# Optimization experiments

Hardware: AMD Instinct MI355X
Metric: run time of the kernel (lower is better)

## Reference

```python
import jax, jax.numpy as jnp
import numpy as np

# dims
N_USER = 30000; N_ITEM = 30000; HID = 256; HEADS = 4; DH = HID // HEADS
L = 2; E_BUYS = 200000
IMG_D = 512; TASTE_D = 768; NUTR_D = 20; LR = 64; IMG_RANK = 64
EPS = 1e-5
# node type order: 0=user 1=item 2=taste 3=intention 4=image
# edge type order: taste->item, intention->item, image->item, user->item (buys), item->user (bought_by)


def _bn(x, g, b):
    # nn.BatchNorm1d in training mode (biased variance), deterministic
    mu = jnp.mean(x, axis=0)
    var = jnp.mean((x - mu) ** 2, axis=0)
    return (x - mu) * jax.lax.rsqrt(var + EPS) * g + b


def _segment_softmax(logits, seg, n):
    m = jax.ops.segment_max(logits, seg, num_segments=n)
    m = jnp.where(jnp.isfinite(m), m, 0.0)
    e = jnp.exp(logits - m[seg])
    s = jax.ops.segment_sum(e, seg, num_segments=n)
    return e / (s[seg] + 1e-16)


def _model(p, user_id, item_id, buys_src, buys_dst):
    # --- encoders (dropout = identity in eval) ---
    xu = jax.nn.relu(_bn(p['user_emb'][user_id] @ p['user_W'] + p['user_b'], p['user_bn_g'], p['user_bn_b']))
    xi = jax.nn.relu(_bn(p['item_emb'][item_id] @ p['item_W'] + p['item_b'], p['item_bn_g'], p['item_bn_b']))
    ximg = (p['image_feat'] @ p['img_U']) @ p['img_V'] + p['img_b']  # LowRankLinear
    xt = p['taste_feat'] @ p['taste_W'] + p['taste_b']
    xn = p['intent_feat'] @ p['intent_W'] + p['intent_b']
    xs = [xu, xi, xt, xn, ximg]
    assoc = jnp.arange(N_ITEM, dtype=jnp.int32)
    # (src_type, dst_type, src_idx, dst_idx)
    edges = [(2, 1, assoc, assoc), (3, 1, assoc, assoc), (4, 1, assoc, assoc),
             (0, 1, buys_src, buys_dst), (1, 0, buys_dst, buys_src)]
    scale = 1.0 / np.sqrt(DH)
    n_of = [N_USER, N_ITEM]
    for l in range(L):
        k, q, v = [], [], []
        for t in range(5):
            kqv = xs[t] @ p['kqv_W'][l, t] + p['kqv_b'][l, t]
            kk, qq, vv = jnp.split(kqv, 3, axis=1)
            k.append(kk.reshape(-1, HEADS, DH))
            q.append(qq.reshape(-1, HEADS, DH))
            v.append(vv.reshape(-1, HEADS, DH))
        buf = {0: [], 1: []}
        for e, (s, d, si, di) in enumerate(edges):
            # relation-specific per-head transforms of source k/v (all src nodes, then gather)
            ke = jnp.einsum('nhd,hde->nhe', k[s], p['k_rel'][l, e])
            ve = jnp.einsum('nhd,hde->nhe', v[s], p['v_rel'][l, e])
            logit = jnp.sum(q[d][di] * ke[si], axis=-1) * p['p_rel'][l, e] * scale  # [E,H]
            buf[d].append((logit, ve[si], di))
        new_xs = list(xs)
        for d in (0, 1):  # dst node types: user, item
            logits = jnp.concatenate([b[0] for b in buf[d]], axis=0)
            msgs = jnp.concatenate([b[1] for b in buf[d]], axis=0)
            dsts = jnp.concatenate([b[2] for b in buf[d]], axis=0)
            alpha = _segment_softmax(logits, dsts, n_of[d])  # softmax over ALL incoming edges per dst node
            agg = jax.ops.segment_sum(alpha[:, :, None] * msgs, dsts, num_segments=n_of[d])
            o = jax.nn.gelu(agg.reshape(-1, HID), approximate=False) @ p['out_W'][l, d] + p['out_b'][l, d]
            sg = jax.nn.sigmoid(p['skip'][l, d])
            o = sg * o + (1.0 - sg) * xs[d]  # HGTConv learned skip
            o = o + xs[d]                    # MultiModalFusionGAT residual
            o = jax.nn.relu(_bn(o, p['fbn_g'][l, d], p['fbn_b'][l, d]))  # per-type BN+ReLU (dropout eval)
            new_xs[d] = o
        xs = new_xs  # taste/intention/image pass through unchanged
    return jnp.stack(xs, axis=0)  # [5, 30000, HID]


def setup_inputs():
    key = jax.random.key(0)
    ks = iter(jax.random.split(key, 48))
    def nrm(shape, scale=0.05):
        return jax.random.normal(next(ks), shape, dtype=jnp.float32) * scale
    z = lambda *s: jnp.zeros(s, jnp.float32)
    o = lambda *s: jnp.ones(s, jnp.float32)
    inp = {}
    inp['user_id'] = jnp.arange(N_USER, dtype=jnp.int32)
    inp['item_id'] = jnp.arange(N_ITEM, dtype=jnp.int32)
    inp['buys_src'] = jax.random.randint(next(ks), (E_BUYS,), 0, N_USER, dtype=jnp.int32)
    inp['buys_dst'] = jax.random.randint(next(ks), (E_BUYS,), 0, N_ITEM, dtype=jnp.int32)
    inp['image_feat'] = nrm((N_ITEM, IMG_D), 1.0)
    inp['taste_feat'] = nrm((N_ITEM, TASTE_D), 1.0)
    inp['intent_feat'] = nrm((N_ITEM, NUTR_D), 1.0)
    inp['user_emb'] = nrm((N_USER, LR), 0.1)
    inp['user_W'] = nrm((LR, HID)); inp['user_b'] = z(HID)
    inp['user_bn_g'] = o(HID); inp['user_bn_b'] = z(HID)
    inp['item_emb'] = nrm((N_ITEM, LR), 0.1)
    inp['item_W'] = nrm((LR, HID)); inp['item_b'] = z(HID)
    inp['item_bn_g'] = o(HID); inp['item_bn_b'] = z(HID)
    inp['img_U'] = nrm((IMG_D, IMG_RANK)); inp['img_V'] = nrm((IMG_RANK, HID)); inp['img_b'] = z(HID)
    inp['taste_W'] = nrm((TASTE_D, HID)); inp['taste_b'] = z(HID)
    inp['intent_W'] = nrm((NUTR_D, HID)); inp['intent_b'] = z(HID)
    inp['kqv_W'] = nrm((L, 5, HID, 3 * HID)); inp['kqv_b'] = z(L, 5, 3 * HID)
    inp['out_W'] = nrm((L, 5, HID, HID)); inp['out_b'] = z(L, 5, HID)
    inp['k_rel'] = nrm((L, 5, HEADS, DH, DH))
    inp['v_rel'] = nrm((L, 5, HEADS, DH, DH))
    inp['p_rel'] = o(L, 5, HEADS)
    inp['skip'] = o(L, 5)
    inp['fbn_g'] = o(L, 2, HID); inp['fbn_b'] = z(L, 2, HID)
    return inp


def reference(user_id, item_id, buys_src, buys_dst, image_feat, taste_feat, intent_feat,
              user_emb, user_W, user_b, user_bn_g, user_bn_b,
              item_emb, item_W, item_b, item_bn_g, item_bn_b,
              img_U, img_V, img_b, taste_W, taste_b, intent_W, intent_b,
              kqv_W, kqv_b, out_W, out_b, k_rel, v_rel, p_rel, skip, fbn_g, fbn_b):
    p = dict(image_feat=image_feat, taste_feat=taste_feat, intent_feat=intent_feat,
             user_emb=user_emb, user_W=user_W, user_b=user_b, user_bn_g=user_bn_g, user_bn_b=user_bn_b,
             item_emb=item_emb, item_W=item_W, item_b=item_b, item_bn_g=item_bn_g, item_bn_b=item_bn_b,
             img_U=img_U, img_V=img_V, img_b=img_b, taste_W=taste_W, taste_b=taste_b,
             intent_W=intent_W, intent_b=intent_b, kqv_W=kqv_W, kqv_b=kqv_b, out_W=out_W, out_b=out_b,
             k_rel=k_rel, v_rel=v_rel, p_rel=p_rel, skip=skip, fbn_g=fbn_g, fbn_b=fbn_b)
    return _model(p, user_id, item_id, buys_src, buys_dst)
```

## Files before the change

kernel.cpp:

```cpp
#include <hip/hip_runtime.h>
#include <math.h>

#define HID 256
#define EBUY 200000
#define NNODE 30000
#define MPD 30208
static const size_t S  = (size_t)NNODE * HID;
static const size_t SP = (size_t)MPD * HID;

typedef __attribute__((ext_vector_type(8))) short  short8;
typedef __attribute__((ext_vector_type(4))) float  f32x4;

#define OFF_TASTE 0
#define OFF_INT   196608
#define OFF_IMGU  204800
#define OFF_IMGV  237568
#define OFF_USER  253952
#define OFF_ITEM  270336
#define OFF_OUTW  286720
#define WENC_TOT  548864

__device__ __forceinline__ float gelu_f(float x) {
    return 0.5f * x * (1.0f + erff(x * 0.70710678118654752f));
}
__device__ __forceinline__ unsigned short f2bf(float f) {
    unsigned u = __float_as_uint(f);
    u = (u + 0x7FFFu + ((u >> 16) & 1u)) >> 16;
    return (unsigned short)u;
}
__device__ __forceinline__ float b2f(unsigned short us) {
    return __uint_as_float((unsigned)us << 16);
}
__device__ __forceinline__ void gl_lds16(const unsigned short* g, unsigned short* l) {
    __builtin_amdgcn_global_load_lds(
        (const __attribute__((address_space(1))) unsigned int*)g,
        (__attribute__((address_space(3))) unsigned int*)l, 16, 0, 0);
}
__device__ __forceinline__ int xcd_swz(int bid, int nwg) {
    int q = nwg >> 3, r = nwg & 7;
    int xc = bid & 7, i = bid >> 3;
    int base = (xc < r) ? xc * (q + 1) : r * (q + 1) + (xc - r) * q;
// ... 121 lines not shown
        for (int j = 0; j < 4; ++j) acc[i][j] = zero;

    const int lrow = lane >> 2, lchk = lane & 3;
    const int gsw = (lchk ^ ((lrow >> 1) & 3)) * 8;
    int cB0 = min(col0 + wid * 32 + lrow, N - 1);
    int cB1 = min(col0 + wid * 32 + 16 + lrow, N - 1);
    const unsigned short* Bp0 = BT + (size_t)cB0 * K + gsw;
    const unsigned short* Bp1 = BT + (size_t)cB1 * K + gsw;
    const int ofs0 = wid * 1024, ofs1 = wid * 1024 + 512;

    const unsigned short* Ap0b = nullptr; const unsigned short* Ap1b = nullptr;
    const float* Af0 = nullptr; const float* Af1 = nullptr;
    const int rA0 = tid >> 2, rA1 = (tid >> 2) + 64;
    const int q0 = tid & 3;
    const int wsw = (q0 ^ ((rA0 >> 1) & 3)) * 8;
    if (GATH2) {
        int lr0 = row0 + rA0 - tt * MPD; if (lr0 >= NNODE) lr0 = NNODE - 1;
        int lr1 = row0 + rA1 - tt * MPD; if (lr1 >= NNODE) lr1 = NNODE - 1;
        const int* gA = tt ? g2 : g1;
        const float* Abase = tt ? (const float*)Ap2 : (const float*)Ap;
        Af0 = Abase + (size_t)gA[lr0] * K;
        Af1 = Abase + (size_t)gA[lr1] * K;
    } else if (AF32) {
        Af0 = (const float*)Ap + (size_t)min(row0 + rA0, M - 1) * K;
        Af1 = (const float*)Ap + (size_t)min(row0 + rA1, M - 1) * K;
    } else {
        int rr0 = min(row0 + wid * 32 + lrow, M - 1);
        int rr1 = min(row0 + wid * 32 + 16 + lrow, M - 1);
        Ap0b = (const unsigned short*)Ap + (size_t)rr0 * K + gsw;
        Ap1b = (const unsigned short*)Ap + (size_t)rr1 * K + gsw;
    }

    const int nt = K >> 5;
    int cur = 0;
    const int rsw = ((l16 >> 1) & 3);

    #define STAGE_F32(c, k0) do { \
        float4 x0 = *(const float4*)&Af0[(k0) + q0 * 8]; \
        float4 x1 = *(const float4*)&Af0[(k0) + q0 * 8 + 4]; \
        float4 y0 = *(const float4*)&Af1[(k0) + q0 * 8]; \
        float4 y1 = *(const float4*)&Af1[(k0) + q0 * 8 + 4]; \
        ushort4 u0 = {f2bf(x0.x), f2bf(x0.y), f2bf(x0.z), f2bf(x0.w)}; \
        ushort4 u1 = {f2bf(x1.x), f2bf(x1.y), f2bf(x1.z), f2bf(x1.w)}; \
        ushort4 w0 = {f2bf(y0.x), f2bf(y0.y), f2bf(y0.z), f2bf(y0.w)}; \
        ushort4 w1 = {f2bf(y1.x), f2bf(y1.y), f2bf(y1.z), f2bf(y1.w)}; \
        *(ushort4*)&sm.AB[c][rA0 * 32 + wsw]     = u0; \
        *(ushort4*)&sm.AB[c][rA0 * 32 + wsw + 4] = u1; \
        *(ushort4*)&sm.AB[c][rA1 * 32 + wsw]     = w0; \
        *(ushort4*)&sm.AB[c][rA1 * 32 + wsw + 4] = w1; \
        gl_lds16(Bp0 + (k0), &sm.AB[2 + (c)][ofs0]); \
        gl_lds16(Bp1 + (k0), &sm.AB[2 + (c)][ofs1]); \
    } while (0)

    #define STAGE_A(c, k0) do { \
        gl_lds16(Ap0b + (k0), &sm.AB[c][ofs0]); \
        gl_lds16(Ap1b + (k0), &sm.AB[c][ofs1]); \
        gl_lds16(Bp0 + (k0), &sm.AB[2 + (c)][ofs0]); \
        gl_lds16(Bp1 + (k0), &sm.AB[2 + (c)][ofs1]); \
    } while (0)

    #define LOADFRAG(c) do { \
        _Pragma("unroll") \
        for (int i = 0; i < 4; ++i) { \
            af[i]  = *(const short8*)&sm.AB[c][(wr * 64 + i * 16 + l16) * 32 + (kg ^ rsw) * 8]; \
            bfr[i] = *(const short8*)&sm.AB[2 + (c)][(wc * 64 + i * 16 + l16) * 32 + (kg ^ rsw) * 8]; \
        } \
    } while (0)

    #define MMAS() do { \
        _Pragma("unroll") \
        for (int i = 0; i < 4; ++i) \
            _Pragma("unroll") \
            for (int j = 0; j < 4; ++j) \
                acc[i][j] = __builtin_amdgcn_mfma_f32_16x16x32_bf16(af[i], bfr[j], acc[i][j], 0, 0, 0); \
    } while (0)

    if (AF32 || GATH2) {
        STAGE_F32(0, 0);
        __syncthreads();
        for (int s = 0; s < nt; ++s) {
            if (s + 1 < nt) STAGE_F32(cur ^ 1, (s + 1) * 32);
            short8 af[4], bfr[4];
            LOADFRAG(cur);
            MMAS();
            __syncthreads();
            cur ^= 1;
        }
    } else {
        STAGE_A(0, 0);
        for (int s = 0; s < nt; ++s) {
            if (s + 1 < nt) {
                STAGE_A(cur ^ 1, (s + 1) * 32);
                asm volatile("s_waitcnt vmcnt(4)" ::: "memory");
            } else {
                asm volatile("s_waitcnt vmcnt(0)" ::: "memory");
            }
            __builtin_amdgcn_s_barrier();
            asm volatile("" ::: "memory");
            short8 af[4], bfr[4];
            LOADFRAG(cur);
            __builtin_amdgcn_s_setprio(1);
            MMAS();
            __builtin_amdgcn_s_setprio(0);
            __builtin_amdgcn_s_barrier();
            asm volatile("" ::: "memory");
            cur ^= 1;
        }
    }
    #undef STAGE_F32
    #undef STAGE_A
    #undef LOADFRAG
    #undef MMAS

    #pragma unroll
    for (int j = 0; j < 4; ++j) {
        int lc = wc * 64 + j * 16 + l16;
        int cc = col0 + lc;
        float bv = (bias && cc < N) ? bias[cc] : 0.f;
        #pragma unroll
        for (int i = 0; i < 4; ++i) {
            #pragma unroll
            for (int r = 0; r < 4; ++r) {
// ... 11 lines not shown
    }
    if (EPI == 0) {
        __syncthreads();
        int nloc = N - col0; if (nloc > 128) nloc = 128;
        if (nloc >= 128) {
            int lr = tid >> 1, half = tid & 1;
            int rr = row0 + lr;
            if (rr < M) {
                uint4* dst = (uint4*)&Db[(size_t)rr * N + col0 + half * 64];
                #pragma unroll
                for (int c = 0; c < 8; ++c) {
                    int ch = half * 8 + c;
                    dst[c] = *(const uint4*)&sm.O[lr * 128 + ((ch ^ (lr & 7)) << 3)];
                }
            }
        } else {
            if (tid < 128) {
                int lr = tid, rr = row0 + lr;
                if (rr < M) {
                    uint4* dst = (uint4*)&Db[(size_t)rr * N + col0];
                    #pragma unroll
                    for (int c = 0; c < 8; ++c)
                        dst[c] = *(const uint4*)&sm.O[lr * 128 + ((c ^ (lr & 7)) << 3)];
                }
            }
        }
    }
}

__launch_bounds__(256)
__global__ void gemm_kvq768(const unsigned short* __restrict__ A,
                            const unsigned short* __restrict__ WALLl,
                            const float* __restrict__ bALLl,
                            unsigned short* __restrict__ KE,
                            unsigned short* __restrict__ VE,
                            unsigned short* __restrict__ QB)
{
    __shared__ union {
        unsigned short AB[4][4096];
        unsigned short O[16384];
    } sm;
    const int tid = threadIdx.x;
    int f = xcd_swz(blockIdx.x, 5664);
    int tt, bx, by;
    if (f < 2832) { tt = f / 1416; int r = f % 1416; by = r / 6; bx = r % 6; }
    else          { int g = f - 2832; tt = 2 + g / 944; int r = g % 944; by = r / 4; bx = r % 4; }
    const int row0 = by * 128, col0 = bx * 128;
    const int wid = tid >> 6, lane = tid & 63;
    const int wr = wid >> 1, wc = wid & 1;
    const int l16 = lane & 15, kg = lane >> 4;

    const unsigned short* Ab = A + (size_t)tt * SP;
    const unsigned short* BT = WALLl + (size_t)tt * 196608;
    const float* bias = bALLl + tt * 768;

    f32x4 acc[4][4];
    const f32x4 zero = {0.f, 0.f, 0.f, 0.f};
    #pragma unroll
    for (int i = 0; i < 4; ++i)
        #pragma unroll
        for (int j = 0; j < 4; ++j) acc[i][j] = zero;

    const int lrow = lane >> 2, lchk = lane & 3;
    const int gsw = (lchk ^ ((lrow >> 1) & 3)) * 8;
    const unsigned short* Ap0 = Ab + (size_t)(row0 + wid * 32 + lrow) * 256 + gsw;
    const unsigned short* Ap1 = Ab + (size_t)(row0 + wid * 32 + 16 + lrow) * 256 + gsw;
    const unsigned short* Bp0 = BT + (size_t)(col0 + wid * 32 + lrow) * 256 + gsw;
    const unsigned short* Bp1 = BT + (size_t)(col0 + wid * 32 + 16 + lrow) * 256 + gsw;
    const int ofs0 = wid * 1024, ofs1 = wid * 1024 + 512;
    const int rsw = ((l16 >> 1) & 3);
    int cur = 0;

    #define STAGE_K(c, k0) do { \
        gl_lds16(Ap0 + (k0), &sm.AB[c][ofs0]); \
        gl_lds16(Ap1 + (k0), &sm.AB[c][ofs1]); \
        gl_lds16(Bp0 + (k0), &sm.AB[2 + (c)][ofs0]); \
        gl_lds16(Bp1 + (k0), &sm.AB[2 + (c)][ofs1]); \
    } while (0)

    STAGE_K(0, 0);
    for (int s = 0; s < 8; ++s) {
        if (s + 1 < 8) {
            STAGE_K(cur ^ 1, (s + 1) * 32);
            asm volatile("s_waitcnt vmcnt(4)" ::: "memory");
        } else {
            asm volatile("s_waitcnt vmcnt(0)" ::: "memory");
        }
        __builtin_amdgcn_s_barrier();
        asm volatile("" ::: "memory");
        short8 af[4], bfr[4];
        #pragma unroll
        for (int i = 0; i < 4; ++i) {
            af[i]  = *(const short8*)&sm.AB[cur][(wr * 64 + i * 16 + l16) * 32 + (kg ^ rsw) * 8];
            bfr[i] = *(const short8*)&sm.AB[2 + cur][(wc * 64 + i * 16 + l16) * 32 + (kg ^ rsw) * 8];
        }
        __builtin_amdgcn_s_setprio(1);
        #pragma unroll
        for (int i = 0; i < 4; ++i)
            #pragma unroll
            for (int j = 0; j < 4; ++j)
                acc[i][j] = __builtin_amdgcn_mfma_f32_16x16x32_bf16(af[i], bfr[j], acc[i][j], 0, 0, 0);
        __builtin_amdgcn_s_setprio(0);
        __builtin_amdgcn_s_barrier();
        asm volatile("" ::: "memory");
        cur ^= 1;
    }
    #undef STAGE_K

    #pragma unroll
    for (int j = 0; j < 4; ++j) {
        int lc = wc * 64 + j * 16 + l16;
        float bv = bias[col0 + lc];
        #pragma unroll
        for (int i = 0; i < 4; ++i) {
            #pragma unroll
            for (int r = 0; r < 4; ++r) {
                int lr = wr * 64 + i * 16 + kg * 4 + r;
                float v = acc[i][j][r] + bv;
                sm.O[lr * 128 + ((((lc >> 3) ^ (lr & 7)) << 3) | (lc & 7))] = f2bf(v);
            }
        }
    }
    __syncthreads();
    {
        int dsel = bx >> 1;
        unsigned short* T = ((dsel == 0) ? KE : (dsel == 1) ? VE : QB) + (size_t)tt * SP;
        int cofs = (bx & 1) * 128;
        int lr = tid >> 1, half = tid & 1;
        int rr = row0 + lr;
        uint4* dst = (uint4*)&T[(size_t)rr * 256 + cofs + half * 64];
        #pragma unroll
        for (int c = 0; c < 8; ++c) {
            int ch = half * 8 + c;
            dst[c] = *(const uint4*)&sm.O[lr * 128 + ((ch ^ (lr & 7)) << 3)];
        }
    }
}

__launch_bounds__(256)
__global__ void gemm_outproj(const unsigned short* __restrict__ A,
                             const unsigned short* __restrict__ BT0,
                             const float* __restrict__ bias0,
                             const float* __restrict__ skipB,
                             const float* __restrict__ residB,
                             float* __restrict__ D0, float* __restrict__ bns)
{
    __shared__ unsigned short AB[4][4096];
    const int tid = threadIdx.x;
    int bid = xcd_swz(blockIdx.y * 2 + blockIdx.x, 2 * gridDim.y);
    const int bx = bid % 2, by = bid / 2;
    const int tt = by / 236;
    const int row0 = by * 128, col0 = bx * 128;
    const int row0l = row0 - tt * MPD;
    const int wid = tid >> 6, lane = tid & 63;
    const int wr = wid >> 1, wc = wid & 1;
    const int l16 = lane & 15, kg = lane >> 4;

    const unsigned short* BT = BT0 + (size_t)tt * 65536;
    const float* bias = bias0 + tt * 256;
    const float* resid = residB + (size_t)tt * S;
    float* Dp = D0 + (size_t)tt * SP;
    float* bnp = bns + tt * 512;

    f32x4 acc[4][4];
    const f32x4 zero = {0.f, 0.f, 0.f, 0.f};
    #pragma unroll
    for (int i = 0; i < 4; ++i)
        #pragma unroll
        for (int j = 0; j < 4; ++j) acc[i][j] = zero;

    const int lrow = lane >> 2, lchk = lane & 3;
    const int gsw = (lchk ^ ((lrow >> 1) & 3)) * 8;
    int ar0 = min(row0l + wid * 32 + lrow, NNODE - 1);
    int ar1 = min(row0l + wid * 32 + 16 + lrow, NNODE - 1);
    const unsigned short* Ap0 = A + (size_t)tt * S + (size_t)ar0 * 256 + gsw;
    const unsigned short* Ap1 = A + (size_t)tt * S + (size_t)ar1 * 256 + gsw;
    const unsigned short* Bp0 = BT + (size_t)(col0 + wid * 32 + lrow) * 256 + gsw;
    const unsigned short* Bp1 = BT + (size_t)(col0 + wid * 32 + 16 + lrow) * 256 + gsw;
    const int ofs0 = wid * 1024, ofs1 = wid * 1024 + 512;
    const int rsw = ((l16 >> 1) & 3);
    int cur = 0;

    #define STAGE_O(c, k0) do { \
        gl_lds16(Ap0 + (k0), &AB[c][ofs0]); \
        gl_lds16(Ap1 + (k0), &AB[c][ofs1]); \
        gl_lds16(Bp0 + (k0), &AB[2 + (c)][ofs0]); \
        gl_lds16(Bp1 + (k0), &AB[2 + (c)][ofs1]); \
    } while (0)

    STAGE_O(0, 0);
    for (int s = 0; s < 8; ++s) {
        if (s + 1 < 8) {
            STAGE_O(cur ^ 1, (s + 1) * 32);
            asm volatile("s_waitcnt vmcnt(4)" ::: "memory");
// ... 4 lines not shown
        asm volatile("" ::: "memory");
        short8 af[4], bfr[4];
        #pragma unroll
        for (int i = 0; i < 4; ++i) {
            af[i]  = *(const short8*)&AB[cur][(wr * 64 + i * 16 + l16) * 32 + (kg ^ rsw) * 8];
            bfr[i] = *(const short8*)&AB[2 + cur][(wc * 64 + i * 16 + l16) * 32 + (kg ^ rsw) * 8];
        }
        __builtin_amdgcn_s_setprio(1);
        #pragma unroll
        for (int i = 0; i < 4; ++i)
            #pragma unroll
            for (int j = 0; j < 4; ++j)
                acc[i][j] = __builtin_amdgcn_mfma_f32_16x16x32_bf16(af[i], bfr[j], acc[i][j], 0, 0, 0);
        __builtin_amdgcn_s_setprio(0);
        __builtin_amdgcn_s_barrier();
        asm volatile("" ::: "memory");
        cur ^= 1;
    }
    #undef STAGE_O

    float sg = 1.f / (1.f + __expf(-skipB[tt]));
    #pragma unroll
    for (int j = 0; j < 4; ++j) {
        int cc = col0 + wc * 64 + j * 16 + l16;
        float cs = 0.f, cs2 = 0.f;
        float bv = bias[cc];
        #pragma unroll
        for (int i = 0; i < 4; ++i) {
            #pragma unroll
            for (int r = 0; r < 4; ++r) {
                int lr = row0l + wr * 64 + i * 16 + kg * 4 + r;
                if (lr < NNODE) {
                    float v = acc[i][j][r] + bv;
                    float xo = resid[(size_t)lr * 256 + cc];
                    float o = sg * v + (2.f - sg) * xo;
                    Dp[(size_t)lr * 256 + cc] = o;
                    cs += o; cs2 += o * o;
                }
            }
        }
        cs  += __shfl_xor(cs, 16);  cs  += __shfl_xor(cs, 32);
        cs2 += __shfl_xor(cs2, 16); cs2 += __shfl_xor(cs2, 32);
        if (kg == 0) {
            atomicAdd(&bnp[cc], cs);
            atomicAdd(&bnp[256 + cc], cs2);
        }
    }
}

__global__ void edge_hist2(const int* __restrict__ dstk, const int* __restrict__ srck,
                           int* __restrict__ cnt)
{
    int j = blockIdx.x * 256 + threadIdx.x;
    if (j < EBUY) atomicAdd(&cnt[dstk[j]], 1);
    else if (j < 2 * EBUY) atomicAdd(&cnt[NNODE + srck[j - EBUY]], 1);
}

#define SCAN_NB 30
#define SCAN_CH 1000
__global__ void scan_part(const int* __restrict__ cnt, int* __restrict__ bt)
{
    int set = blockIdx.y;
    const int* c = cnt + set * NNODE;
    int b = blockIdx.x;
    int i = b * SCAN_CH + threadIdx.x;
    int v = (threadIdx.x < SCAN_CH && i < NNODE) ? c[i] : 0;
    __shared__ int wsum[16];
    int lane = threadIdx.x & 63, wv = threadIdx.x >> 6;
    for (int o = 32; o; o >>= 1) v += __shfl_down(v, o);
// ... 31 lines not shown
    int x = v;
    for (int o = 1; o < 64; o <<= 1) { int t = __shfl_up(x, o); if (lane >= o) x += t; }
    __shared__ int wtot[16];
    if (lane == 63) wtot[wv] = x;
    __syncthreads();
    if (wv == 0) {
        int y = (lane < 16) ? wtot[lane] : 0;
        for (int o = 1; o < 16; o <<= 1) { int t = __shfl_up(y, o); if (lane >= o) y += t; }
        if (lane < 16) wtot[lane] = y;
    }
    __syncthreads();
    int wbase = (wv == 0) ? 0 : wtot[wv - 1];
    int excl = bt[set * 32 + b] + wbase + x - v;
    if (threadIdx.x < SCAN_CH && i < NNODE) { off[i] = excl; cur[i] = excl; }
}

__global__ void edge_place2(const int* __restrict__ dstk, const int* __restrict__ srck,
                            int* __restrict__ cur_i, int* __restrict__ cur_u,
                            int* __restrict__ src_i, int* __restrict__ src_u)
{
    int j = blockIdx.x * 256 + threadIdx.x;
    if (j < EBUY) {
        int pos = atomicAdd(&cur_i[dstk[j]], 1);
        src_i[pos] = srck[j];
    } else if (j < 2 * EBUY) {
        int j2 = j - EBUY;
        int pos = atomicAdd(&cur_u[srck[j2]], 1);
        src_u[pos] = dstk[j2];
    }
}

__launch_bounds__(256)
__global__ void attn_both(const unsigned short* __restrict__ QB,
                          const unsigned short* __restrict__ KE,
                          const unsigned short* __restrict__ VE,
                          const int* __restrict__ off_i, const int* __restrict__ src_i,
                          const int* __restrict__ off_u, const int* __restrict__ src_u,
                          const float* __restrict__ pR,
                          unsigned short* __restrict__ AGB)
{
    int gw = (blockIdx.x * 256 + threadIdx.x) >> 6;
    int lane = threadIdx.x & 63;
    if (gw >= 2 * NNODE) return;
    int h = lane >> 4;
    const bool item = gw < NNODE;
    const int wid = item ? gw : gw - NNODE;
    const unsigned short* Qd  = item ? QB + SP : QB;
    const unsigned short* KEs = item ? KE : KE + SP;
    const unsigned short* VEs = item ? VE : VE + SP;
    const int* roff = item ? off_i : off_u;
    const int* srcA = item ? src_i : src_u;
    unsigned short* outp = AGB + (item ? S : 0);

    ushort4 qb = *(const ushort4*)(Qd + (size_t)wid * 256 + lane * 4);
    float4 q = {b2f(qb.x), b2f(qb.y), b2f(qb.z), b2f(qb.w)};
    float m = -INFINITY, s = 0.f;
    float4 acc = {0.f, 0.f, 0.f, 0.f};

    if (item) {
        #pragma unroll
        for (int e = 0; e < 3; ++e) {
            ushort4 kb = *(const ushort4*)(KE + (size_t)(2 + e) * SP + (size_t)wid * 256 + lane * 4);
            float d = q.x * b2f(kb.x) + q.y * b2f(kb.y) + q.z * b2f(kb.z) + q.w * b2f(kb.w);
            for (int off = 8; off; off >>= 1) d += __shfl_xor(d, off, 16);
            float lg = d * pR[e * 4 + h] * 0.125f;
            ushort4 vv = *(const ushort4*)(VE + (size_t)(2 + e) * SP + (size_t)wid * 256 + lane * 4);
            float mn = fmaxf(m, lg);
            float so = __expf(m - mn);
            float ev = __expf(lg - mn);
            s = s * so + ev;
            acc.x = acc.x * so + ev * b2f(vv.x);
            acc.y = acc.y * so + ev * b2f(vv.y);
            acc.z = acc.z * so + ev * b2f(vv.z);
            acc.w = acc.w * so + ev * b2f(vv.w);
            m = mn;
        }
    }

    float pb = pR[(item ? 12 : 16) + h] * 0.125f;
    int j0 = roff[wid], j1 = roff[wid + 1];
    ushort4 kb = {0,0,0,0}, vv = {0,0,0,0};
    if (j0 < j1) {
        int src0 = srcA[j0];
        kb = *(const ushort4*)(KEs + (size_t)src0 * 256 + lane * 4);
        vv = *(const ushort4*)(VEs + (size_t)src0 * 256 + lane * 4);
    }
    for (int j = j0; j < j1; ++j) {
        ushort4 ckb = kb, cvv = vv;
        if (j + 1 < j1) {
            int ns = srcA[j + 1];
            kb = *(const ushort4*)(KEs + (size_t)ns * 256 + lane * 4);
            vv = *(const ushort4*)(VEs + (size_t)ns * 256 + lane * 4);
        }
        float d = q.x * b2f(ckb.x) + q.y * b2f(ckb.y) + q.z * b2f(ckb.z) + q.w * b2f(ckb.w);
        for (int off = 8; off; off >>= 1) d += __shfl_xor(d, off, 16);
        float lg = d * pb;
        float mn = fmaxf(m, lg);
        float so = __expf(m - mn);
        float ev = __expf(lg - mn);
        s = s * so + ev;
        acc.x = acc.x * so + ev * b2f(cvv.x);
        acc.y = acc.y * so + ev * b2f(cvv.y);
        acc.z = acc.z * so + ev * b2f(cvv.z);
        acc.w = acc.w * so + ev * b2f(cvv.w);
        m = mn;
    }

    float inv = 1.f / (s + 1e-16f);
    ushort4 o4;
    o4.x = f2bf(gelu_f(acc.x * inv));
    o4.y = f2bf(gelu_f(acc.y * inv));
    o4.z = f2bf(gelu_f(acc.z * inv));
    o4.w = f2bf(gelu_f(acc.w * inv));
    *(ushort4*)(outp + (size_t)wid * 256 + lane * 4) = o4;
}

#define BNB 512
__global__ void bn_stats2(const float* __restrict__ SCRf, float* __restrict__ part)
{
    int tt = blockIdx.y;
    const float* x = SCRf + (size_t)tt * SP;
    int col = threadIdx.x;
    int b = blockIdx.x;
    float s = 0.f, s2 = 0.f;
    int r = b;
    for (; r + 3 * BNB < NNODE; r += 4 * BNB) {
        float v0 = x[(size_t)r * 256 + col];
        float v1 = x[(size_t)(r + BNB) * 256 + col];
        float v2 = x[(size_t)(r + 2 * BNB) * 256 + col];
        float v3 = x[(size_t)(r + 3 * BNB) * 256 + col];
        s += v0 + v1 + v2 + v3;
        s2 += v0 * v0 + v1 * v1 + v2 * v2 + v3 * v3;
    }
    for (; r < NNODE; r += BNB) {
        float v = x[(size_t)r * 256 + col];
        s += v; s2 += v * v;
    }
    part[((size_t)tt * BNB + b) * 512 + col] = s;
    part[((size_t)tt * BNB + b) * 512 + 256 + col] = s2;
// ... 1 lines not shown

__global__ void bn_fin2(const float* __restrict__ part,
                        const float* __restrict__ g0, const float* __restrict__ b0,
                        const float* __restrict__ g1, const float* __restrict__ b1,
                        float* __restrict__ scsh)
{
    int tid = threadIdx.x;
    int tt = tid >> 8, col = tid & 255;
    const float* p = part + (size_t)tt * BNB * 512;
    float s = 0.f, s2 = 0.f;
    #pragma unroll 4
    for (int b = 0; b < BNB; ++b) { s += p[b * 512 + col]; s2 += p[b * 512 + 256 + col]; }
    float mu = s / (float)NNODE;
    float var = s2 / (float)NNODE - mu * mu;
    float sc = rsqrtf(var + 1e-5f) * (tt ? g1 : g0)[col];
    scsh[tt * 512 + col] = sc;
    scsh[tt * 512 + 256 + col] = (tt ? b1 : b0)[col] - mu * sc;
}

__global__ void bn_find2(const float* __restrict__ bns,
                         const float* __restrict__ g01, const float* __restrict__ b01,
                         float* __restrict__ scsh)
{
    int tid = threadIdx.x;
    int tt = tid >> 8, col = tid & 255;
    float s = bns[tt * 512 + col], s2 = bns[tt * 512 + 256 + col];
    float mu = s / (float)NNODE;
    float var = s2 / (float)NNODE - mu * mu;
    float sc = rsqrtf(var + 1e-5f) * g01[tt * 256 + col];
    scsh[tt * 512 + col] = sc;
    scsh[tt * 512 + 256 + col] = b01[tt * 256 + col] - mu * sc;
}

__global__ void bn_apply2(const float* __restrict__ SCRf, const float* __restrict__ scsh,
                          float* __restrict__ out, unsigned short* __restrict__ XBall)
{
    const int Q4 = NNODE * 64;
    for (int i = blockIdx.x * 256 + threadIdx.x; i < 2 * Q4; i += gridDim.x * 256) {
        int tt = (i >= Q4) ? 1 : 0;
        int local = i - tt * Q4;
        int c4 = local & 63;
        float4 sc4 = *(const float4*)&scsh[tt * 512 + c4 * 4];
        float4 sh4 = *(const float4*)&scsh[tt * 512 + 256 + c4 * 4];
        float4 v = ((const float4*)(SCRf + (size_t)tt * SP))[local];
        v.x = fmaxf(v.x * sc4.x + sh4.x, 0.f);
        v.y = fmaxf(v.y * sc4.y + sh4.y, 0.f);
        v.z = fmaxf(v.z * sc4.z + sh4.z, 0.f);
        v.w = fmaxf(v.w * sc4.w + sh4.w, 0.f);
        ((float4*)(out + (size_t)tt * S))[local] = v;
        ushort4 u = {f2bf(v.x), f2bf(v.y), f2bf(v.z), f2bf(v.w)};
        ((ushort4*)(XBall + (size_t)tt * SP))[local] = u;
    }
}

extern "C" void kernel_launch(void* const* d_in, const int* in_sizes, int n_in,
                              void* d_out, int out_size, void* d_ws, size_t ws_size,
                              hipStream_t stream)
{
    const int*   user_id    = (const int*)d_in[0];
    const int*   item_id    = (const int*)d_in[1];
    const int*   buys_src   = (const int*)d_in[2];
    const int*   buys_dst   = (const int*)d_in[3];
    const float* image_feat = (const float*)d_in[4];
    const float* taste_feat = (const float*)d_in[5];
    const float* intent_feat= (const float*)d_in[6];
    const float* user_emb   = (const float*)d_in[7];
    const float* user_W     = (const float*)d_in[8];
    const float* user_b     = (const float*)d_in[9];
    const float* user_bn_g  = (const float*)d_in[10];
    const float* user_bn_b  = (const float*)d_in[11];
    const float* item_emb   = (const float*)d_in[12];
    const float* item_W     = (const float*)d_in[13];
    const float* item_b     = (const float*)d_in[14];
    const float* item_bn_g  = (const float*)d_in[15];
    const float* item_bn_b  = (const float*)d_in[16];
    const float* img_U      = (const float*)d_in[17];
    const float* img_V      = (const float*)d_in[18];
    const float* img_b      = (const float*)d_in[19];
    const float* taste_W    = (const float*)d_in[20];
    const float* taste_b    = (const float*)d_in[21];
    const float* intent_W   = (const float*)d_in[22];
    const float* intent_b   = (const float*)d_in[23];
    const float* kqv_W      = (const float*)d_in[24];
    const float* kqv_b      = (const float*)d_in[25];
    const float* out_W      = (const float*)d_in[26];
    const float* out_b      = (const float*)d_in[27];
    const float* k_rel      = (const float*)d_in[28];
    const float* v_rel      = (const float*)d_in[29];
    const float* p_rel      = (const float*)d_in[30];
    const float* skip       = (const float*)d_in[31];
    const float* fbn_g      = (const float*)d_in[32];
    const float* fbn_b      = (const float*)d_in[33];

    float* out = (float*)d_out;
    float* ws  = (float*)d_ws;

    float* SCRf = ws;
    float* BNSp = SCRf + 2 * SP;
    float* BNS  = BNSp + 2 * BNB * 512;
    float* SCSH = BNS + 1024;
    float* bALL = SCSH + 1024;
    unsigned short* QB    = (unsigned short*)(bALL + 7680);
    unsigned short* XBall = QB + 2 * SP;
    unsigned short* KEall = XBall + 5 * SP;
    unsigned short* VEall = KEall + 5 * SP;
    unsigned short* AGB   = VEall + 5 * SP;
    unsigned short* IMB   = AGB + 2 * S;
    unsigned short* IPB   = IMB + (size_t)NNODE * 64;
    unsigned short* WALL  = IPB + (size_t)NNODE * 32;
    unsigned short* WENC  = WALL + (size_t)10 * 196608;
    int* cnt   = (int*)(WENC + WENC_TOT);
    int* off_i = cnt + 2 * NNODE;
    int* off_u = off_i + NNODE + 1;
    int* cur_i = off_u + NNODE + 1;
    int* cur_u = cur_i + NNODE;
    int* src_i = cur_u + NNODE;
    int* src_u = src_i + EBUY;
    int* bt    = src_u + EBUY;

    size_t need = (size_t)((char*)(bt + 64) - (char*)ws);
    if (ws_size < need) return;

    unsigned short* TFB = (unsigned short*)SCRf;
    unsigned short* IFB = QB;

    hipMemsetAsync(cnt, 0, 2 * NNODE * 4, stream);
    edge_hist2<<<(2 * EBUY + 255) / 256, 256, 0, stream>>>(buys_dst, buys_src, cnt);
    scan_part<<<dim3(SCAN_NB, 2), 1024, 0, stream>>>(cnt, bt);
    scan_mid<<<1, 64, 0, stream>>>(bt, off_i, off_u);
    scan_final<<<dim3(SCAN_NB, 2), 1024, 0, stream>>>(cnt, bt, off_i, off_u, cur_i, cur_u);
    edge_place2<<<(2 * EBUY + 255) / 256, 256, 0, stream>>>(buys_dst, buys_src, cur_i, cur_u, src_i, src_u);

    wtconv_all<<<(WENC_TOT + 255) / 256, 256, 0, stream>>>(taste_W, intent_W, img_U, img_V,
                                                           user_W, item_W, out_W, WENC);
    build_kqv<<<dim3(771, 10), 256, 0, stream>>>(kqv_W, kqv_b, k_rel, v_rel, WALL, bALL);
    conv_pad<<<(NNODE * 32 + 255) / 256, 256, 0, stream>>>(intent_feat, IPB, NNODE, 20, 32);
    conv2bf<<<2048, 256, 0, stream>>>(taste_feat, 5760000, TFB, image_feat, 3840000, IFB);

    hipLaunchKernelGGL((gemm_mfma<0,0,0>), dim3(2,235), dim3(256), 0, stream,
        TFB, nullptr, nullptr, nullptr, WENC + OFF_TASTE, taste_b, nullptr,
        out + 2*S, XBall + 2*SP, NNODE, 256, 768);
    hipLaunchKernelGGL((gemm_mfma<0,0,0>), dim3(2,235), dim3(256), 0, stream,
        IPB, nullptr, nullptr, nullptr, WENC + OFF_INT, intent_b, nullptr,
        out + 3*S, XBall + 3*SP, NNODE, 256, 32);
    hipLaunchKernelGGL((gemm_mfma<0,0,0>), dim3(1,235), dim3(256), 0, stream,
        IFB, nullptr, nullptr, nullptr, WENC + OFF_IMGU, nullptr, nullptr,
        nullptr, IMB, NNODE, 64, 512);
    hipLaunchKernelGGL((gemm_mfma<0,0,0>), dim3(2,235), dim3(256), 0, stream,
        IMB, nullptr, nullptr, nullptr, WENC + OFF_IMGV, img_b, nullptr,
        out + 4*S, XBall + 4*SP, NNODE, 256, 64);
    hipLaunchKernelGGL((gemm_mfma<1,1,6>), dim3(2,472), dim3(256), 0, stream,
        user_emb, item_emb, user_id, item_id, WENC + OFF_USER, user_b, item_b,
        SCRf, nullptr, 2*MPD, 256, 64);
    bn_stats2<<<dim3(BNB, 2), 256, 0, stream>>>(SCRf, BNSp);
    bn_fin2<<<1, 512, 0, stream>>>(BNSp, user_bn_g, user_bn_b, item_bn_g, item_bn_b, SCSH);
    bn_apply2<<<960, 256, 0, stream>>>(SCRf, SCSH, out, XBall);

    for (int l = 0; l < 2; ++l) {
        hipLaunchKernelGGL(gemm_kvq768, dim3(5664), dim3(256), 0, stream,
            XBall, WALL + (size_t)l*5*196608, bALL + l*5*768, KEall, VEall, QB);
        hipLaunchKernelGGL(attn_both, dim3((2*NNODE*64 + 255)/256), dim3(256), 0, stream,
            QB, KEall, VEall, off_i, src_i, off_u, src_u, p_rel + l*20, AGB);
        hipMemsetAsync(BNS, 0, 1024 * 4, stream);
        hipLaunchKernelGGL(gemm_outproj, dim3(2, 472), dim3(256), 0, stream,
            AGB, WENC + OFF_OUTW + (size_t)l*2*65536, out_b + (size_t)l*5*256,
            skip + l*5, out, SCRf, BNS);
        bn_find2<<<1, 512, 0, stream>>>(BNS, fbn_g + (size_t)l*2*256, fbn_b + (size_t)l*2*256, SCSH);
        bn_apply2<<<960, 256, 0, stream>>>(SCRf, SCSH, out, XBall);
    }
}
```

Measured before the change: 962.5 us.

## Use BK=64 in KQV GEMM and read bf16 residual instead of fp32 output

The KQV GEMM now stages 64-wide K tiles with an 8-chunk XOR swizzle. That halves the number of loop iterations and barriers, at the cost of doubling LDS per block, which may lower occupancy. The output-projection residual is read from the bf16 activation buffer rather than the fp32 output. BN-apply skips the fp32 output write except on the final layer, which cuts memory traffic but feeds the residual at reduced precision.

```diff
diff --git a/kernel.cpp b/kernel.cpp
--- a/kernel.cpp
+++ b/kernel.cpp
@@ -194,7 +194,6 @@
     }
 
     const int nt = K >> 5;
-    int cur = 0;
     const int rsw = ((l16 >> 1) & 3);
 
     #define STAGE_F32(c, k0) do { \
@@ -240,6 +239,7 @@
     if (AF32 || GATH2) {
         STAGE_F32(0, 0);
         __syncthreads();
+        int cur = 0;
         for (int s = 0; s < nt; ++s) {
             if (s + 1 < nt) STAGE_F32(cur ^ 1, (s + 1) * 32);
             short8 af[4], bfr[4];
@@ -250,6 +250,7 @@
         }
     } else {
         STAGE_A(0, 0);
+        int cur = 0;
         for (int s = 0; s < nt; ++s) {
             if (s + 1 < nt) {
                 STAGE_A(cur ^ 1, (s + 1) * 32);
@@ -332,7 +333,7 @@
                             unsigned short* __restrict__ QB)
 {
     __shared__ union {
-        unsigned short AB[4][4096];
+        unsigned short AB[4][8192];
         unsigned short O[16384];
     } sm;
     const int tid = threadIdx.x;
@@ -356,45 +357,55 @@
         #pragma unroll
         for (int j = 0; j < 4; ++j) acc[i][j] = zero;
 
-    const int lrow = lane >> 2, lchk = lane & 3;
-    const int gsw = (lchk ^ ((lrow >> 1) & 3)) * 8;
-    const unsigned short* Ap0 = Ab + (size_t)(row0 + wid * 32 + lrow) * 256 + gsw;
-    const unsigned short* Ap1 = Ab + (size_t)(row0 + wid * 32 + 16 + lrow) * 256 + gsw;
-    const unsigned short* Bp0 = BT + (size_t)(col0 + wid * 32 + lrow) * 256 + gsw;
-    const unsigned short* Bp1 = BT + (size_t)(col0 + wid * 32 + 16 + lrow) * 256 + gsw;
-    const int ofs0 = wid * 1024, ofs1 = wid * 1024 + 512;
-    const int rsw = ((l16 >> 1) & 3);
+    const int lrow8 = lane >> 3, lchk8 = lane & 7;
+    const unsigned short* ApL[4];
+    const unsigned short* BpL[4];
+    #pragma unroll
+    for (int q = 0; q < 4; ++q) {
+        int ar = wid * 32 + q * 8 + lrow8;
+        ApL[q] = Ab + (size_t)(row0 + ar) * 256 + (size_t)((lchk8 ^ (ar & 7)) << 3);
+        int bc = wid * 32 + q * 8 + lrow8;
+        BpL[q] = BT + (size_t)(col0 + bc) * 256 + (size_t)((lchk8 ^ (bc & 7)) << 3);
+    }
+    const int sofs = wid * 2048;
+
+    #define STAGE_K(c, k0) do { \
+        _Pragma("unroll") \
+        for (int q = 0; q < 4; ++q) gl_lds16(ApL[q] + (k0), &sm.AB[c][sofs + q * 512]); \
+        _Pragma("unroll") \
+        for (int q = 0; q < 4; ++q) gl_lds16(BpL[q] + (k0), &sm.AB[2 + (c)][sofs + q * 512]); \
+    } while (0)
+
+    STAGE_K(0, 0);
     int cur = 0;
-
-    #define STAGE_K(c, k0) do { \
-        gl_lds16(Ap0 + (k0), &sm.AB[c][ofs0]); \
-        gl_lds16(Ap1 + (k0), &sm.AB[c][ofs1]); \
-        gl_lds16(Bp0 + (k0), &sm.AB[2 + (c)][ofs0]); \
-        gl_lds16(Bp1 + (k0), &sm.AB[2 + (c)][ofs1]); \
-    } while (0)
-
-    STAGE_K(0, 0);
-    for (int s = 0; s < 8; ++s) {
-        if (s + 1 < 8) {
-            STAGE_K(cur ^ 1, (s + 1) * 32);
-            asm volatile("s_waitcnt vmcnt(4)" ::: "memory");
+    for (int s = 0; s < 4; ++s) {
+        if (s + 1 < 4) {
+            STAGE_K(cur ^ 1, (s + 1) * 64);
+            asm volatile("s_waitcnt vmcnt(8)" ::: "memory");
         } else {
             asm volatile("s_waitcnt vmcnt(0)" ::: "memory");
         }
         __builtin_amdgcn_s_barrier();
         asm volatile("" ::: "memory");
-        short8 af[4], bfr[4];
-        #pragma unroll
-        for (int i = 0; i < 4; ++i) {
-            af[i]  = *(const short8*)&sm.AB[cur][(wr * 64 + i * 16 + l16) * 32 + (kg ^ rsw) * 8];
-            bfr[i] = *(const short8*)&sm.AB[2 + cur][(wc * 64 + i * 16 + l16) * 32 + (kg ^ rsw) * 8];
+        short8 af[2][4], bfr[2][4];
+        #pragma unroll
+        for (int kk = 0; kk < 2; ++kk) {
+            #pragma unroll
+            for (int i = 0; i < 4; ++i) {
+                int ar = wr * 64 + i * 16 + l16;
+                af[kk][i] = *(const short8*)&sm.AB[cur][ar * 64 + (((kk * 4 + kg) ^ (ar & 7)) << 3)];
+                int bc = wc * 64 + i * 16 + l16;
+                bfr[kk][i] = *(const short8*)&sm.AB[2 + cur][bc * 64 + (((kk * 4 + kg) ^ (bc & 7)) << 3)];
+            }
         }
         __builtin_amdgcn_s_setprio(1);
         #pragma unroll
-        for (int i = 0; i < 4; ++i)
+        for (int kk = 0; kk < 2; ++kk)
             #pragma unroll
-            for (int j = 0; j < 4; ++j)
-                acc[i][j] = __builtin_amdgcn_mfma_f32_16x16x32_bf16(af[i], bfr[j], acc[i][j], 0, 0, 0);
+            for (int i = 0; i < 4; ++i)
+                #pragma unroll
+                for (int j = 0; j < 4; ++j)
+                    acc[i][j] = __builtin_amdgcn_mfma_f32_16x16x32_bf16(af[kk][i], bfr[kk][j], acc[i][j], 0, 0, 0);
         __builtin_amdgcn_s_setprio(0);
         __builtin_amdgcn_s_barrier();
         asm volatile("" ::: "memory");
@@ -437,7 +448,7 @@
                              const unsigned short* __restrict__ BT0,
                              const float* __restrict__ bias0,
                              const float* __restrict__ skipB,
-                             const float* __restrict__ residB,
+                             const unsigned short* __restrict__ XBres,
                              float* __restrict__ D0, float* __restrict__ bns)
 {
     __shared__ unsigned short AB[4][4096];
@@ -453,7 +464,7 @@
 
     const unsigned short* BT = BT0 + (size_t)tt * 65536;
     const float* bias = bias0 + tt * 256;
-    const float* resid = residB + (size_t)tt * S;
+    const unsigned short* resid = XBres + (size_t)tt * SP;
     float* Dp = D0 + (size_t)tt * SP;
     float* bnp = bns + tt * 512;
 
@@ -525,7 +536,7 @@
                 int lr = row0l + wr * 64 + i * 16 + kg * 4 + r;
                 if (lr < NNODE) {
                     float v = acc[i][j][r] + bv;
-                    float xo = resid[(size_t)lr * 256 + cc];
+                    float xo = b2f(resid[(size_t)lr * 256 + cc]);
                     float o = sg * v + (2.f - sg) * xo;
                     Dp[(size_t)lr * 256 + cc] = o;
                     cs += o; cs2 += o * o;
@@ -765,6 +776,7 @@
     scsh[tt * 512 + 256 + col] = b01[tt * 256 + col] - mu * sc;
 }
 
+template<int WF32>
 __global__ void bn_apply2(const float* __restrict__ SCRf, const float* __restrict__ scsh,
                           float* __restrict__ out, unsigned short* __restrict__ XBall)
 {
@@ -780,7 +792,7 @@
         v.y = fmaxf(v.y * sc4.y + sh4.y, 0.f);
         v.z = fmaxf(v.z * sc4.z + sh4.z, 0.f);
         v.w = fmaxf(v.w * sc4.w + sh4.w, 0.f);
-        ((float4*)(out + (size_t)tt * S))[local] = v;
+        if (WF32) ((float4*)(out + (size_t)tt * S))[local] = v;
         ushort4 u = {f2bf(v.x), f2bf(v.y), f2bf(v.z), f2bf(v.w)};
         ((ushort4*)(XBall + (size_t)tt * SP))[local] = u;
     }
@@ -887,7 +899,7 @@
         SCRf, nullptr, 2*MPD, 256, 64);
     bn_stats2<<<dim3(BNB, 2), 256, 0, stream>>>(SCRf, BNSp);
     bn_fin2<<<1, 512, 0, stream>>>(BNSp, user_bn_g, user_bn_b, item_bn_g, item_bn_b, SCSH);
-    bn_apply2<<<960, 256, 0, stream>>>(SCRf, SCSH, out, XBall);
+    bn_apply2<0><<<960, 256, 0, stream>>>(SCRf, SCSH, out, XBall);
 
     for (int l = 0; l < 2; ++l) {
         hipLaunchKernelGGL(gemm_kvq768, dim3(5664), dim3(256), 0, stream,
@@ -897,8 +909,9 @@
         hipMemsetAsync(BNS, 0, 1024 * 4, stream);
         hipLaunchKernelGGL(gemm_outproj, dim3(2, 472), dim3(256), 0, stream,
             AGB, WENC + OFF_OUTW + (size_t)l*2*65536, out_b + (size_t)l*5*256,
-            skip + l*5, out, SCRf, BNS);
+            skip + l*5, XBall, SCRf, BNS);
         bn_find2<<<1, 512, 0, stream>>>(BNS, fbn_g + (size_t)l*2*256, fbn_b + (size_t)l*2*256, SCSH);
-        bn_apply2<<<960, 256, 0, stream>>>(SCRf, SCSH, out, XBall);
-    }
-}
+        if (l == 0) bn_apply2<0><<<960, 256, 0, stream>>>(SCRf, SCSH, out, XBall);
+        else        bn_apply2<1><<<960, 256, 0, stream>>>(SCRf, SCSH, out, XBall);
+    }
+}
```

Result: faster. 916.6 us (-4.8%).

## Interleave K/V rows, keep residual and outproj in bf16, skip intermediate fp32 writes

Applied to the files above, without the earlier changes.

K and V projections are now stored interleaved in one 512-wide row per node, so each attention edge gather reads one contiguous row instead of two separate buffers. The attention loop also prefetches two edges ahead. The out-projection reads its residual from the bf16 activation buffer and writes bf16 instead of fp32, and the fp32 output tensor is written only in the final layer's BN apply. Together these cut memory traffic, at the cost of extra bf16 rounding on the residual and on the pre-BN activations.

```diff
diff --git a/kernel.cpp b/kernel.cpp
--- a/kernel.cpp
+++ b/kernel.cpp
@@ -5,8 +5,9 @@
 #define EBUY 200000
 #define NNODE 30000
 #define MPD 30208
-static const size_t S  = (size_t)NNODE * HID;
-static const size_t SP = (size_t)MPD * HID;
+static const size_t S   = (size_t)NNODE * HID;
+static const size_t SP  = (size_t)MPD * HID;
+static const size_t SP2 = (size_t)MPD * 512;
 
 typedef __attribute__((ext_vector_type(8))) short  short8;
 typedef __attribute__((ext_vector_type(4))) float  f32x4;
@@ -194,7 +195,6 @@
     }
 
     const int nt = K >> 5;
-    int cur = 0;
     const int rsw = ((l16 >> 1) & 3);
 
     #define STAGE_F32(c, k0) do { \
@@ -240,6 +240,7 @@
     if (AF32 || GATH2) {
         STAGE_F32(0, 0);
         __syncthreads();
+        int cur = 0;
         for (int s = 0; s < nt; ++s) {
             if (s + 1 < nt) STAGE_F32(cur ^ 1, (s + 1) * 32);
             short8 af[4], bfr[4];
@@ -250,6 +251,7 @@
         }
     } else {
         STAGE_A(0, 0);
+        int cur = 0;
         for (int s = 0; s < nt; ++s) {
             if (s + 1 < nt) {
                 STAGE_A(cur ^ 1, (s + 1) * 32);
@@ -327,8 +329,7 @@
 __global__ void gemm_kvq768(const unsigned short* __restrict__ A,
                             const unsigned short* __restrict__ WALLl,
                             const float* __restrict__ bALLl,
-                            unsigned short* __restrict__ KE,
-                            unsigned short* __restrict__ VE,
+                            unsigned short* __restrict__ KV,
                             unsigned short* __restrict__ QB)
 {
     __shared__ union {
@@ -419,11 +420,12 @@
     __syncthreads();
     {
         int dsel = bx >> 1;
-        unsigned short* T = ((dsel == 0) ? KE : (dsel == 1) ? VE : QB) + (size_t)tt * SP;
-        int cofs = (bx & 1) * 128;
+        unsigned short* T; int ldT, cofs;
+        if (dsel == 2) { T = QB + (size_t)tt * SP;  ldT = 256; cofs = (bx & 1) * 128; }
+        else           { T = KV + (size_t)tt * SP2; ldT = 512; cofs = dsel * 256 + (bx & 1) * 128; }
         int lr = tid >> 1, half = tid & 1;
         int rr = row0 + lr;
-        uint4* dst = (uint4*)&T[(size_t)rr * 256 + cofs + half * 64];
+        uint4* dst = (uint4*)&T[(size_t)rr * ldT + cofs + half * 64];
         #pragma unroll
         for (int c = 0; c < 8; ++c) {
             int ch = half * 8 + c;
@@ -437,8 +439,8 @@
                              const unsigned short* __restrict__ BT0,
                              const float* __restrict__ bias0,
                              const float* __restrict__ skipB,
-                             const float* __restrict__ residB,
-                             float* __restrict__ D0, float* __restrict__ bns)
+                             const unsigned short* __restrict__ XBres,
+                             unsigned short* __restrict__ Db, float* __restrict__ bns)
 {
     __shared__ unsigned short AB[4][4096];
     const int tid = threadIdx.x;
@@ -453,8 +455,8 @@
 
     const unsigned short* BT = BT0 + (size_t)tt * 65536;
     const float* bias = bias0 + tt * 256;
-    const float* resid = residB + (size_t)tt * S;
-    float* Dp = D0 + (size_t)tt * SP;
+    const unsigned short* resid = XBres + (size_t)tt * SP;
+    unsigned short* Dp = Db + (size_t)tt * SP;
     float* bnp = bns + tt * 512;
 
     f32x4 acc[4][4];
@@ -525,9 +527,9 @@
                 int lr = row0l + wr * 64 + i * 16 + kg * 4 + r;
                 if (lr < NNODE) {
                     float v = acc[i][j][r] + bv;
-                    float xo = resid[(size_t)lr * 256 + cc];
+                    float xo = b2f(resid[(size_t)lr * 256 + cc]);
                     float o = sg * v + (2.f - sg) * xo;
-                    Dp[(size_t)lr * 256 + cc] = o;
+                    Dp[(size_t)lr * 256 + cc] = f2bf(o);
                     cs += o; cs2 += o * o;
                 }
             }
@@ -625,8 +627,7 @@
 
 __launch_bounds__(256)
 __global__ void attn_both(const unsigned short* __restrict__ QB,
-                          const unsigned short* __restrict__ KE,
-                          const unsigned short* __restrict__ VE,
+                          const unsigned short* __restrict__ KV,
                           const int* __restrict__ off_i, const int* __restrict__ src_i,
                           const int* __restrict__ off_u, const int* __restrict__ src_u,
                           const float* __restrict__ pR,
@@ -639,8 +640,7 @@
     const bool item = gw < NNODE;
     const int wid = item ? gw : gw - NNODE;
     const unsigned short* Qd  = item ? QB + SP : QB;
-    const unsigned short* KEs = item ? KE : KE + SP;
-    const unsigned short* VEs = item ? VE : VE + SP;
+    const unsigned short* KVs = item ? KV : KV + SP2;
     const int* roff = item ? off_i : off_u;
     const int* srcA = item ? src_i : src_u;
     unsigned short* outp = AGB + (item ? S : 0);
@@ -650,54 +650,65 @@
     float m = -INFINITY, s = 0.f;
     float4 acc = {0.f, 0.f, 0.f, 0.f};
 
+    #define AT_STEP(KBV, VBV, PSCALE) do { \
+        float d = q.x * b2f((KBV).x) + q.y * b2f((KBV).y) + q.z * b2f((KBV).z) + q.w * b2f((KBV).w); \
+        for (int off = 8; off; off >>= 1) d += __shfl_xor(d, off, 16); \
+        float lg = d * (PSCALE); \
+        float mn = fmaxf(m, lg); \
+        float so = __expf(m - mn); \
+        float ev = __expf(lg - mn); \
+        s = s * so + ev; \
+        acc.x = acc.x * so + ev * b2f((VBV).x); \
+        acc.y = acc.y * so + ev * b2f((VBV).y); \
+        acc.z = acc.z * so + ev * b2f((VBV).z); \
+        acc.w = acc.w * so + ev * b2f((VBV).w); \
+        m = mn; \
+    } while (0)
+
     if (item) {
         #pragma unroll
         for (int e = 0; e < 3; ++e) {
-            ushort4 kb = *(const ushort4*)(KE + (size_t)(2 + e) * SP + (size_t)wid * 256 + lane * 4);
-            float d = q.x * b2f(kb.x) + q.y * b2f(kb.y) + q.z * b2f(kb.z) + q.w * b2f(kb.w);
-            for (int off = 8; off; off >>= 1) d += __shfl_xor(d, off, 16);
-            float lg = d * pR[e * 4 + h] * 0.125f;
-            ushort4 vv = *(const ushort4*)(VE + (size_t)(2 + e) * SP + (size_t)wid * 256 + lane * 4);
-            float mn = fmaxf(m, lg);
-            float so = __expf(m - mn);
-            float ev = __expf(lg - mn);
-            s = s * so + ev;
-            acc.x = acc.x * so + ev * b2f(vv.x);
-            acc.y = acc.y * so + ev * b2f(vv.y);
-            acc.z = acc.z * so + ev * b2f(vv.z);
-            acc.w = acc.w * so + ev * b2f(vv.w);
-            m = mn;
+            const unsigned short* kvrow = KV + (size_t)(2 + e) * SP2 + (size_t)wid * 512;
+            ushort4 kb = *(const ushort4*)(kvrow + lane * 4);
+            ushort4 vv = *(const ushort4*)(kvrow + 256 + lane * 4);
+            AT_STEP(kb, vv, pR[e * 4 + h] * 0.125f);
         }
     }
 
     float pb = pR[(item ? 12 : 16) + h] * 0.125f;
     int j0 = roff[wid], j1 = roff[wid + 1];
-    ushort4 kb = {0,0,0,0}, vv = {0,0,0,0};
+    ushort4 kA = {0,0,0,0}, vA = {0,0,0,0}, kB = {0,0,0,0}, vB = {0,0,0,0};
     if (j0 < j1) {
-        int src0 = srcA[j0];
-        kb = *(const ushort4*)(KEs + (size_t)src0 * 256 + lane * 4);
-        vv = *(const ushort4*)(VEs + (size_t)src0 * 256 + lane * 4);
-    }
-    for (int j = j0; j < j1; ++j) {
-        ushort4 ckb = kb, cvv = vv;
-        if (j + 1 < j1) {
-            int ns = srcA[j + 1];
-            kb = *(const ushort4*)(KEs + (size_t)ns * 256 + lane * 4);
-            vv = *(const ushort4*)(VEs + (size_t)ns * 256 + lane * 4);
-        }
-        float d = q.x * b2f(ckb.x) + q.y * b2f(ckb.y) + q.z * b2f(ckb.z) + q.w * b2f(ckb.w);
-        for (int off = 8; off; off >>= 1) d += __shfl_xor(d, off, 16);
-        float lg = d * pb;
-        float mn = fmaxf(m, lg);
-        float so = __expf(m - mn);
-        float ev = __expf(lg - mn);
-        s = s * so + ev;
-        acc.x = acc.x * so + ev * b2f(cvv.x);
-        acc.y = acc.y * so + ev * b2f(cvv.y);
-        acc.z = acc.z * so + ev * b2f(cvv.z);
-        acc.w = acc.w * so + ev * b2f(cvv.w);
-        m = mn;
-    }
+        const unsigned short* r0 = KVs + (size_t)srcA[j0] * 512;
+        kA = *(const ushort4*)(r0 + lane * 4);
+        vA = *(const ushort4*)(r0 + 256 + lane * 4);
+    }
+    if (j0 + 1 < j1) {
+        const unsigned short* r1 = KVs + (size_t)srcA[j0 + 1] * 512;
+        kB = *(const ushort4*)(r1 + lane * 4);
+        vB = *(const ushort4*)(r1 + 256 + lane * 4);
+    }
+    int j = j0;
+    while (j < j1) {
+        ushort4 ck = kA, cv = vA;
+        if (j + 2 < j1) {
+            const unsigned short* rn = KVs + (size_t)srcA[j + 2] * 512;
+            kA = *(const ushort4*)(rn + lane * 4);
+            vA = *(const ushort4*)(rn + 256 + lane * 4);
+        }
+        AT_STEP(ck, cv, pb);
+        ++j;
+        if (j >= j1) break;
+        ck = kB; cv = vB;
+        if (j + 2 < j1) {
+            const unsigned short* rn = KVs + (size_t)srcA[j + 2] * 512;
+            kB = *(const ushort4*)(rn + lane * 4);
+            vB = *(const ushort4*)(rn + 256 + lane * 4);
+        }
+        AT_STEP(ck, cv, pb);
+        ++j;
+    }
+    #undef AT_STEP
 
     float inv = 1.f / (s + 1e-16f);
     ushort4 o4;
@@ -765,6 +776,7 @@
     scsh[tt * 512 + 256 + col] = b01[tt * 256 + col] - mu * sc;
 }
 
+template<int WF32>
 __global__ void bn_apply2(const float* __restrict__ SCRf, const float* __restrict__ scsh,
                           float* __restrict__ out, unsigned short* __restrict__ XBall)
 {
@@ -780,7 +792,30 @@
         v.y = fmaxf(v.y * sc4.y + sh4.y, 0.f);
         v.z = fmaxf(v.z * sc4.z + sh4.z, 0.f);
         v.w = fmaxf(v.w * sc4.w + sh4.w, 0.f);
-        ((float4*)(out + (size_t)tt * S))[local] = v;
+        if (WF32) ((float4*)(out + (size_t)tt * S))[local] = v;
+        ushort4 u = {f2bf(v.x), f2bf(v.y), f2bf(v.z), f2bf(v.w)};
+        ((ushort4*)(XBall + (size_t)tt * SP))[local] = u;
+    }
+}
+
+template<int WF32>
+__global__ void bn_apply2b(const unsigned short* __restrict__ SCRb, const float* __restrict__ scsh,
+                           float* __restrict__ out, unsigned short* __restrict__ XBall)
+{
+    const int Q4 = NNODE * 64;
+    for (int i = blockIdx.x * 256 + threadIdx.x; i < 2 * Q4; i += gridDim.x * 256) {
+        int tt = (i >= Q4) ? 1 : 0;
+        int local = i - tt * Q4;
+        int c4 = local & 63;
+        float4 sc4 = *(const float4*)&scsh[tt * 512 + c4 * 4];
+        float4 sh4 = *(const float4*)&scsh[tt * 512 + 256 + c4 * 4];
+        ushort4 b4 = ((const ushort4*)(SCRb + (size_t)tt * SP))[local];
+        float4 v = {b2f(b4.x), b2f(b4.y), b2f(b4.z), b2f(b4.w)};
+        v.x = fmaxf(v.x * sc4.x + sh4.x, 0.f);
+        v.y = fmaxf(v.y * sc4.y + sh4.y, 0.f);
+        v.z = fmaxf(v.z * sc4.z + sh4.z, 0.f);
+        v.w = fmaxf(v.w * sc4.w + sh4.w, 0.f);
+        if (WF32) ((float4*)(out + (size_t)tt * S))[local] = v;
         ushort4 u = {f2bf(v.x), f2bf(v.y), f2bf(v.z), f2bf(v.w)};
         ((ushort4*)(XBall + (size_t)tt * SP))[local] = u;
     }
@@ -835,9 +870,8 @@
     float* bALL = SCSH + 1024;
     unsigned short* QB    = (unsigned short*)(bALL + 7680);
     unsigned short* XBall = QB + 2 * SP;
-    unsigned short* KEall = XBall + 5 * SP;
-    unsigned short* VEall = KEall + 5 * SP;
-    unsigned short* AGB   = VEall + 5 * SP;
+    unsigned short* KVall = XBall + 5 * SP;
+    unsigned short* AGB   = KVall + 5 * SP2;
     unsigned short* IMB   = AGB + 2 * S;
     unsigned short* IPB   = IMB + (size_t)NNODE * 64;
     unsigned short* WALL  = IPB + (size_t)NNODE * 32;
@@ -854,8 +888,9 @@
     size_t need = (size_t)((char*)(bt + 64) - (char*)ws);
     if (ws_size < need) return;
 
-    unsigned short* TFB = (unsigned short*)SCRf;
-    unsigned short* IFB = QB;
+    unsigned short* TFB  = (unsigned short*)SCRf;
+    unsigned short* IFB  = QB;
+    unsigned short* SCRb = (unsigned short*)SCRf;
 
     hipMemsetAsync(cnt, 0, 2 * NNODE * 4, stream);
     edge_hist2<<<(2 * EBUY + 255) / 256, 256, 0, stream>>>(buys_dst, buys_src, cnt);
@@ -887,18 +922,19 @@
         SCRf, nullptr, 2*MPD, 256, 64);
     bn_stats2<<<dim3(BNB, 2), 256, 0, stream>>>(SCRf, BNSp);
     bn_fin2<<<1, 512, 0, stream>>>(BNSp, user_bn_g, user_bn_b, item_bn_g, item_bn_b, SCSH);
-    bn_apply2<<<960, 256, 0, stream>>>(SCRf, SCSH, out, XBall);
+    bn_apply2<0><<<960, 256, 0, stream>>>(SCRf, SCSH, out, XBall);
 
     for (int l = 0; l < 2; ++l) {
         hipLaunchKernelGGL(gemm_kvq768, dim3(5664), dim3(256), 0, stream,
-            XBall, WALL + (size_t)l*5*196608, bALL + l*5*768, KEall, VEall, QB);
+            XBall, WALL + (size_t)l*5*196608, bALL + l*5*768, KVall, QB);
         hipLaunchKernelGGL(attn_both, dim3((2*NNODE*64 + 255)/256), dim3(256), 0, stream,
-            QB, KEall, VEall, off_i, src_i, off_u, src_u, p_rel + l*20, AGB);
+            QB, KVall, off_i, src_i, off_u, src_u, p_rel + l*20, AGB);
         hipMemsetAsync(BNS, 0, 1024 * 4, stream);
         hipLaunchKernelGGL(gemm_outproj, dim3(2, 472), dim3(256), 0, stream,
             AGB, WENC + OFF_OUTW + (size_t)l*2*65536, out_b + (size_t)l*5*256,
-            skip + l*5, out, SCRf, BNS);
+            skip + l*5, XBall, SCRb, BNS);
         bn_find2<<<1, 512, 0, stream>>>(BNS, fbn_g + (size_t)l*2*256, fbn_b + (size_t)l*2*256, SCSH);
-        bn_apply2<<<960, 256, 0, stream>>>(SCRf, SCSH, out, XBall);
-    }
-}
+        if (l == 0) bn_apply2b<0><<<960, 256, 0, stream>>>(SCRb, SCSH, out, XBall);
+        else        bn_apply2b<1><<<960, 256, 0, stream>>>(SCRb, SCSH, out, XBall);
+    }
+}
```

Measured after the change: 882.8 us (median of 2 runs). 1.09x faster.
